# Performance work log

Hardware: AMD Instinct MI355X
Metric: run time of the kernel (lower is better)

## Reference

```python
import jax, jax.numpy as jnp
import numpy as np

DIM = 2048
N_HEADS = 16
HEAD_DIM = 128
EPS = 1e-6


def setup_inputs() -> dict:
    key = jax.random.key(0)
    ks = jax.random.split(key, 8)
    b, gf, gh, gw = 1, 8, 16, 24
    s = gf * gh * gw
    c = HEAD_DIM // 2
    w = lambda k: 0.02 * jax.random.normal(k, (DIM, DIM), jnp.float32)
    return {
        "x": jax.random.normal(ks[0], (b, s, DIM), jnp.float32),
        "freqs_angle": jax.random.normal(ks[1], (1024, c), jnp.float32),
        "Wq": w(ks[2]), "bq": jnp.zeros((DIM,), jnp.float32),
        "Wk": w(ks[3]), "bk": jnp.zeros((DIM,), jnp.float32),
        "Wv": w(ks[4]), "bv": jnp.zeros((DIM,), jnp.float32),
        "Wo": w(ks[5]), "bo": jnp.zeros((DIM,), jnp.float32),
        "gq": jnp.ones((DIM,), jnp.float32),
        "gk": jnp.ones((DIM,), jnp.float32),
        "seq_len": s, "grid_f": gf, "grid_h": gh, "grid_w": gw,
    }


def _rms(t, g):
    return t * jax.lax.rsqrt(jnp.mean(t * t, axis=-1, keepdims=True) + EPS) * g


def _grid_angles(freqs_angle, gf, gh, gw, c):
    # band split [c - 2*(c//3), c//3, c//3] as in rope_apply
    cf = c - 2 * (c // 3)
    ch = cw = c // 3
    af = freqs_angle[:gf, :cf]            # [F, cf]
    ah = freqs_angle[:gh, cf:cf + ch]     # [H, ch]
    aw = freqs_angle[:gw, cf + ch:c]      # [W, cw]
    ang = jnp.concatenate([
        jnp.broadcast_to(af[:, None, None, :], (gf, gh, gw, cf)),
        jnp.broadcast_to(ah[None, :, None, :], (gf, gh, gw, ch)),
        jnp.broadcast_to(aw[None, None, :, :], (gf, gh, gw, cw)),
    ], axis=-1)
    return ang.reshape(gf * gh * gw, c)   # [s, c]


def reference(x, freqs_angle, Wq, bq, Wk, bk, Wv, bv, Wo, bo, gq, gk,
              seq_len, grid_f, grid_h, grid_w):
    b, s, _ = x.shape
    n, d = N_HEADS, HEAD_DIM
    c = d // 2
    ang = _grid_angles(freqs_angle, grid_f, grid_h, grid_w, c)
    cos = jnp.cos(ang)[None, :, None, :]  # [1, s, 1, c]
    sin = jnp.sin(ang)[None, :, None, :]

    def rope(t):  # complex multiply on (even, odd) = (real, imag) pairs
        te, to = t[..., 0::2], t[..., 1::2]
        return jnp.stack([te * cos - to * sin, te * sin + to * cos], axis=-1).reshape(t.shape)

    q = _rms(x @ Wq.T + bq, gq).reshape(b, s, n, d)
    k = _rms(x @ Wk.T + bk, gk).reshape(b, s, n, d)
    v = (x @ Wv.T + bv).reshape(b, s, n, d)
    q, k = rope(q), rope(k)

    scale = np.float32(1.0 / np.sqrt(d))
    scores = jnp.einsum('bqnd,bknd->bnqk', q, k) * scale
    p = jax.nn.softmax(scores, axis=-1)
    o = jnp.einsum('bnqk,bknd->bqnd', p, v).reshape(b, s, n * d)
    return o @ Wo.T + bo
```

## Files before the change

kernel.cpp:

```cpp
#include <hip/hip_runtime.h>
#include <stdint.h>
#include <stddef.h>

typedef __bf16 bf16_t;
typedef __bf16 bf16x8 __attribute__((ext_vector_type(8)));
typedef __bf16 bf16x4 __attribute__((ext_vector_type(4)));
typedef __bf16 bf16x2 __attribute__((ext_vector_type(2)));
typedef float  f32x4  __attribute__((ext_vector_type(4)));
typedef float  f32x16 __attribute__((ext_vector_type(16)));

#define SEQ   3072
#define DIMD  2048
#define NH    16
#define HD    128
#define QKVN  6144

__device__ __forceinline__ void async16(const bf16_t* g, bf16_t* l) {
  __builtin_amdgcn_global_load_lds((const __attribute__((address_space(1))) uint32_t*)g,
                                   (__attribute__((address_space(3))) uint32_t*)l, 16, 0, 0);
}

__global__ __launch_bounds__(256) void cvt_all(const float* __restrict__ x,
                                               const float* __restrict__ Wq,
                                               const float* __restrict__ Wk,
                                               const float* __restrict__ Wv,
                                               const float* __restrict__ Wo,
                                               const float* __restrict__ bq,
                                               const float* __restrict__ bk,
                                               const float* __restrict__ bv,
                                               bf16_t* __restrict__ xb,
                                               bf16_t* __restrict__ Wqkvb,
                                               bf16_t* __restrict__ Wob,
                                               float* __restrict__ bqkv) {
  const int b = blockIdx.x;
  const float* src; bf16_t* dst; int off;
  if (b < 3072)       { src = x;  dst = xb;              off = b; }
  else if (b < 5120)  { src = Wq; dst = Wqkvb;           off = b - 3072; }
  else if (b < 7168)  { src = Wk; dst = Wqkvb + 4194304; off = b - 5120; }
  else if (b < 9216)  { src = Wv; dst = Wqkvb + 8388608; off = b - 7168; }
  else if (b < 11264) { src = Wo; dst = Wob;             off = b - 9216; }
  else {
    int t = (b - 11264) * 256 + threadIdx.x;
    float v;
    if (t < 2048)      v = bq[t];
    else if (t < 4096) v = bk[t - 2048];
    else               v = bv[t - 4096];
    bqkv[t] = v;
    return;
  }
  const int idx = (off * 256 + threadIdx.x) * 8;
  const float4 a = *(const float4*)(src + idx);
  const float4 c = *(const float4*)(src + idx + 4);
  bf16x8 o;
  o[0] = (bf16_t)a.x; o[1] = (bf16_t)a.y; o[2] = (bf16_t)a.z; o[3] = (bf16_t)a.w;
  o[4] = (bf16_t)c.x; o[5] = (bf16_t)c.y; o[6] = (bf16_t)c.z; o[7] = (bf16_t)c.w;
  *(bf16x8*)(dst + idx) = o;
}

template<bool OUT_BF16>
__global__ __launch_bounds__(256, 2) void gemm_nt(const bf16_t* __restrict__ A,
                                                  const bf16_t* __restrict__ B,
                                                  const float* __restrict__ bias,
                                                  void* __restrict__ Cout,
                                                  int M, int N, int K) {
  __shared__ __align__(16) bf16_t As[128 * 64];
  __shared__ __align__(16) bf16_t Bs[128 * 64];
  const int t = threadIdx.x;
  const int lane = t & 63, wave = t >> 6;
  const int quad = lane >> 4, l15 = lane & 15;
  const int wy = wave >> 1, wx = wave & 1;
  const size_t bm = (size_t)blockIdx.y * 128, bn = (size_t)blockIdx.x * 128;
  const bf16_t* Ab = A + bm * K;
  const bf16_t* Bb = B + bn * K;
  f32x4 acc[4][4] = {};
  int srow[4], scol[4];
#pragma unroll
  for (int r = 0; r < 4; r++) {
    int L = r * 256 + t;
    int row = L >> 3, cp = L & 7;
    srow[r] = row;
    scol[r] = (cp ^ (row & 7)) * 8;
  }
  for (int k0 = 0; k0 < K; k0 += 64) {
    __syncthreads();
#pragma unroll
    for (int r = 0; r < 4; r++)
      async16(Ab + (size_t)srow[r] * K + k0 + scol[r], &As[(r * 256 + t) * 8]);
#pragma unroll
    for (int r = 0; r < 4; r++)
      async16(Bb + (size_t)srow[r] * K + k0 + scol[r], &Bs[(r * 256 + t) * 8]);
    __syncthreads();
#pragma unroll
    for (int ks = 0; ks < 2; ks++) {
      bf16x8 af[4], bfv[4];
#pragma unroll
      for (int i = 0; i < 4; i++) {
        int row = wy * 64 + i * 16 + l15;
        af[i] = *(const bf16x8*)&As[row * 64 + (((ks * 4 + quad) ^ (row & 7)) * 8)];
      }
#pragma unroll
      for (int j = 0; j < 4; j++) {
        int row = wx * 64 + j * 16 + l15;
        bfv[j] = *(const bf16x8*)&Bs[row * 64 + (((ks * 4 + quad) ^ (row & 7)) * 8)];
      }
#pragma unroll
      for (int i = 0; i < 4; i++)
#pragma unroll
        for (int j = 0; j < 4; j++)
          acc[i][j] = __builtin_amdgcn_mfma_f32_16x16x32_bf16(af[i], bfv[j], acc[i][j], 0, 0, 0);
    }
  }
#pragma unroll
  for (int i = 0; i < 4; i++) {
#pragma unroll
    for (int j = 0; j < 4; j++) {
      size_t row = bm + wy * 64 + i * 16 + quad * 4;
      size_t col = bn + wx * 64 + j * 16 + l15;
      float bb = bias[col];
#pragma unroll
      for (int r = 0; r < 4; r++) {
        float v = acc[i][j][r] + bb;
        if (OUT_BF16) ((bf16_t*)Cout)[(row + r) * N + col] = (bf16_t)v;
        else          ((float*)Cout)[(row + r) * N + col] = v;
      }
    }
  }
}

__global__ __launch_bounds__(256) void rmsrope(bf16_t* __restrict__ qkv,
                                               bf16_t* __restrict__ pk,
                                               const float* __restrict__ gq,
                                               const float* __restrict__ gk,
                                               const float* __restrict__ freqs) {
  const int s = blockIdx.x, t = threadIdx.x;
  bf16_t* row = qkv + (size_t)s * QKVN;
  bf16x8 qv = *(const bf16x8*)&row[t * 8];
  bf16x8 kv = *(const bf16x8*)&row[2048 + t * 8];
  float qf[8], kf[8];
  float qs = 0.f, ks2 = 0.f;
#pragma unroll
  for (int i = 0; i < 8; i++) {
    qf[i] = (float)qv[i]; qs  += qf[i] * qf[i];
    kf[i] = (float)kv[i]; ks2 += kf[i] * kf[i];
  }
#pragma unroll
  for (int m = 1; m < 64; m <<= 1) {
    qs  += __shfl_xor(qs, m);
    ks2 += __shfl_xor(ks2, m);
  }
  __shared__ float red[2][4];
  const int wave = t >> 6, lane = t & 63;
  if (lane == 0) { red[0][wave] = qs; red[1][wave] = ks2; }
  __syncthreads();
  qs  = red[0][0] + red[0][1] + red[0][2] + red[0][3];
  ks2 = red[1][0] + red[1][1] + red[1][2] + red[1][3];
  const float qsc = rsqrtf(qs  / 2048.f + 1e-6f) * 0.12751745f;
  const float ksc = rsqrtf(ks2 / 2048.f + 1e-6f);
  const int sf = s / 384, rem = s - sf * 384;
  const int sh = rem / 24, sw = rem - sh * 24;
  bf16x8 qo, ko;
#pragma unroll
  for (int u = 0; u < 4; u++) {
    const int col = t * 8 + 2 * u;
    const int i = (col >> 1) & 63;
    const int frow = (i < 22) ? sf : ((i < 43) ? sh : sw);
    const float ang = freqs[frow * 64 + i];
    float sn, cs;
    __sincosf(ang, &sn, &cs);
    float te = qf[2 * u]     * qsc * gq[col];
    float to = qf[2 * u + 1] * qsc * gq[col + 1];
    qo[2 * u]     = (bf16_t)(te * cs - to * sn);
    qo[2 * u + 1] = (bf16_t)(te * sn + to * cs);
    te = kf[2 * u]     * ksc * gk[col];
    to = kf[2 * u + 1] * ksc * gk[col + 1];
    ko[2 * u]     = (bf16_t)(te * cs - to * sn);
    ko[2 * u + 1] = (bf16_t)(te * sn + to * cs);
  }
  *(bf16x8*)&row[t * 8] = qo;
  *(bf16x8*)&pk[((size_t)(t >> 4) * SEQ + s) * HD + (t & 15) * 8] = ko;
}

__global__ __launch_bounds__(256) void vtrans(const bf16_t* __restrict__ qkv,
                                              bf16_t* __restrict__ pvt) {
  __shared__ bf16_t tile[128][65];
  const int h = blockIdx.y;
  const int s0 = blockIdx.x * 64;
  const int t = threadIdx.x;
#pragma unroll
  for (int r = 0; r < 4; r++) {
    int L = r * 256 + t, s = L >> 4, cp = L & 15;
    bf16x8 v = *(const bf16x8*)&qkv[(size_t)(s0 + s) * QKVN + 4096 + h * HD + cp * 8];
#pragma unroll
    for (int i = 0; i < 8; i++) tile[cp * 8 + i][s] = v[i];
  }
  __syncthreads();
#pragma unroll
  for (int r = 0; r < 4; r++) {
    int L = r * 256 + t, d = L >> 3, c = L & 7;
    bf16x8 o;
#pragma unroll
    for (int i = 0; i < 8; i++) o[i] = tile[d][c * 8 + i];
    *(bf16x8*)&pvt[((size_t)h * HD + d) * SEQ + s0 + c * 8] = o;
  }
}

#define STAGE_KV(BUF, KV1) do {                                              \
    _Pragma("unroll")                                                        \
    for (int r = 0; r < 5; r++) {                                            \
      int L = r * 192 + t;                                                   \
      async16(pkh + (size_t)(KV1) * HD + koff[r], &Ks[BUF][L * 8]);          \
      async16(pvh + (KV1) + voff[r], &Vt[BUF][L * 8]);                       \
    }                                                                        \
    if (t < 64) {                                                            \
      int L = 5 * 192 + t;                                                   \
      async16(pkh + (size_t)(KV1) * HD + koff[5], &Ks[BUF][L * 8]);          \
      async16(pvh + (KV1) + voff[5], &Vt[BUF][L * 8]);                       \
    }                                                                        \
  } while (0)

__global__ __launch_bounds__(192, 2) void flash_attn(const bf16_t* __restrict__ qkv,
                                                     const bf16_t* __restrict__ pk,
                                                     const bf16_t* __restrict__ pvt,
                                                     bf16_t* __restrict__ ob) {
  __shared__ __align__(16) bf16_t Ks[2][64 * 128];
  __shared__ __align__(16) bf16_t Vt[2][128 * 64];
  const int hh = blockIdx.y, qt = blockIdx.x;
  const int s0 = qt * 96;
  const int t = threadIdx.x, wave = t >> 6, lane = t & 63;
  const int l31 = lane & 31, hl = lane >> 5;
  const int wq = wave * 32;
  const bf16_t* pkh = pk  + (size_t)hh * (SEQ * HD);
  const bf16_t* pvh = pvt + (size_t)hh * (HD * SEQ);
  int koff[6], voff[6];
#pragma unroll
  for (int r = 0; r < 6; r++) {
    int L = r * 192 + t;
    int krow = L >> 4, kc = (L & 15) ^ (krow & 7);
    koff[r] = krow * HD + kc * 8;
    int vd = L >> 3, vc = (L & 7) ^ (vd & 7);
    voff[r] = vd * SEQ + vc * 8;
  }
  bf16x8 qfr[8];
#pragma unroll
  for (int ks = 0; ks < 8; ks++)
    qfr[ks] = *(const bf16x8*)&qkv[(size_t)(s0 + wq + l31) * QKVN + hh * HD + ks * 16 + hl * 8];
  bf16x8 vones;
#pragma unroll
  for (int i = 0; i < 8; i++) vones[i] = (bf16_t)1.0f;
  f32x16 oacc[4] = {};
  f32x16 lacc = {};
  float m_run = -3e38f;
  STAGE_KV(0, 0);
  for (int kt = 0; kt < SEQ / 64; kt++) {
    const int cur = kt & 1;
    __syncthreads();
    if (kt + 1 < SEQ / 64) STAGE_KV(cur ^ 1, (kt + 1) * 64);
    f32x16 st0 = {}, st1 = {};
    __builtin_amdgcn_s_setprio(1);
#pragma unroll
    for (int ks = 0; ks < 8; ks++) {
      const int r1 = 32 + l31;
      bf16x8 k0 = *(const bf16x8*)&Ks[cur][l31 * 128 + (((ks * 2 + hl) ^ (l31 & 7)) * 8)];
      bf16x8 k1 = *(const bf16x8*)&Ks[cur][r1 * 128 + (((ks * 2 + hl) ^ (r1 & 7)) * 8)];
      st0 = __builtin_amdgcn_mfma_f32_32x32x16_bf16(k0, qfr[ks], st0, 0, 0, 0);
      st1 = __builtin_amdgcn_mfma_f32_32x32x16_bf16(k1, qfr[ks], st1, 0, 0, 0);
    }
    __builtin_amdgcn_s_setprio(0);
    float mt = st0[0];
#pragma unroll
    for (int r = 1; r < 16; r++) mt = fmaxf(mt, st0[r]);
#pragma unroll
    for (int r = 0; r < 16; r++) mt = fmaxf(mt, st1[r]);
    mt = fmaxf(mt, __shfl_xor(mt, 32));
    if (!__all(mt <= m_run + 11.5f)) {
      const float mn = fmaxf(m_run, mt);
      const float al = __builtin_amdgcn_exp2f(m_run - mn);
      m_run = mn;
#pragma unroll
      for (int r = 0; r < 16; r++) {
        const float a = __shfl(al, (r & 3) + 8 * (r >> 2) + 4 * hl);
        lacc[r] *= a;
#pragma unroll
        for (int dj = 0; dj < 4; dj++) oacc[dj][r] *= a;
      }
    }
    uint32_t c0[8], c1[8];
#pragma unroll
    for (int m = 0; m < 8; m++) {
      bf16x2 w0, w1;
      w0[0] = (bf16_t)__builtin_amdgcn_exp2f(st0[2 * m]     - m_run);
      w0[1] = (bf16_t)__builtin_amdgcn_exp2f(st0[2 * m + 1] - m_run);
      w1[0] = (bf16_t)__builtin_amdgcn_exp2f(st1[2 * m]     - m_run);
      w1[1] = (bf16_t)__builtin_amdgcn_exp2f(st1[2 * m + 1] - m_run);
      c0[m] = __builtin_bit_cast(uint32_t, w0);
      c1[m] = __builtin_bit_cast(uint32_t, w1);
    }
    union U8 { uint32_t u[4]; bf16x8 v; } afr0, afr1, afr2, afr3;
#define BUILD_AFR(DST, CB, B) do {                                           \
      uint32_t sA = hl ? CB[(B) + 0] : CB[(B) + 2];                          \
      uint32_t sB = hl ? CB[(B) + 1] : CB[(B) + 3];                          \
      uint32_t rA = (uint32_t)__shfl_xor((int)sA, 32);                       \
      uint32_t rB = (uint32_t)__shfl_xor((int)sB, 32);                       \
      DST.u[0] = hl ? rA : CB[(B) + 0];                                      \
      DST.u[1] = hl ? rB : CB[(B) + 1];                                      \
      DST.u[2] = hl ? CB[(B) + 2] : rA;                                      \
      DST.u[3] = hl ? CB[(B) + 3] : rB;                                      \
    } while (0)
    BUILD_AFR(afr0, c0, 0);
    BUILD_AFR(afr1, c0, 4);
    BUILD_AFR(afr2, c1, 0);
    BUILD_AFR(afr3, c1, 4);
#undef BUILD_AFR
    __builtin_amdgcn_s_setprio(1);
#define PV_STEP(AFR, S) do {                                                            \
      lacc = __builtin_amdgcn_mfma_f32_32x32x16_bf16(AFR.v, vones, lacc, 0, 0, 0);      \
      _Pragma("unroll")                                                                 \
      for (int dj = 0; dj < 4; dj++) {                                                  \
        const int row = dj * 32 + l31;                                                  \
        bf16x8 vf = *(const bf16x8*)&Vt[cur][row * 64 + ((((S) * 2 + hl) ^ (row & 7)) * 8)]; \
        oacc[dj] = __builtin_amdgcn_mfma_f32_32x32x16_bf16(AFR.v, vf, oacc[dj], 0, 0, 0);    \
      }                                                                                 \
    } while (0)
    PV_STEP(afr0, 0);
    PV_STEP(afr1, 1);
    PV_STEP(afr2, 2);
    PV_STEP(afr3, 3);
#undef PV_STEP
    __builtin_amdgcn_s_setprio(0);
  }
#pragma unroll
  for (int r = 0; r < 16; r++) {
    const float li = 1.f / lacc[r];
    const size_t row = (size_t)(s0 + wq + (r & 3) + 8 * (r >> 2) + 4 * hl);
#pragma unroll
    for (int dj = 0; dj < 4; dj++)
      ob[row * DIMD + hh * HD + dj * 32 + l31] = (bf16_t)(oacc[dj][r] * li);
  }
}

extern "C" void kernel_launch(void* const* d_in, const int* in_sizes, int n_in,
                              void* d_out, int out_size, void* d_ws, size_t ws_size,
                              hipStream_t stream) {
  (void)in_sizes; (void)n_in; (void)out_size;
  const float* x     = (const float*)d_in[0];
  const float* freqs = (const float*)d_in[1];
  const float* Wq    = (const float*)d_in[2];
  const float* bq    = (const float*)d_in[3];
  const float* Wk    = (const float*)d_in[4];
  const float* bk    = (const float*)d_in[5];
  const float* Wv    = (const float*)d_in[6];
  const float* bv    = (const float*)d_in[7];
  const float* Wo    = (const float*)d_in[8];
  const float* bo    = (const float*)d_in[9];
  const float* gq    = (const float*)d_in[10];
  const float* gk    = (const float*)d_in[11];

  char* w = (char*)d_ws;
  bf16_t* xb    = (bf16_t*)(w);
  bf16_t* Wqkvb = (bf16_t*)(w + 12582912);
  bf16_t* Wob   = (bf16_t*)(w + 37748736);
  bf16_t* qkvb  = (bf16_t*)(w + 46137344);
  bf16_t* obuf  = (bf16_t*)(w + 83886080);
  float*  bqkv  = (float*) (w + 96468992);
  bf16_t* pk    = (bf16_t*)(w);
  bf16_t* pvt   = (bf16_t*)(w + 12582912);
  if (ws_size < (size_t)96493568) return;

  cvt_all<<<11288, 256, 0, stream>>>(x, Wq, Wk, Wv, Wo, bq, bk, bv, xb, Wqkvb, Wob, bqkv);

  gemm_nt<true><<<dim3(48, 24), 256, 0, stream>>>(xb, Wqkvb, bqkv, qkvb, SEQ, QKVN, DIMD);
  rmsrope<<<3072, 256, 0, stream>>>(qkvb, pk, gq, gk, freqs);
  vtrans<<<dim3(48, NH), 256, 0, stream>>>(qkvb, pvt);
  flash_attn<<<dim3(32, NH), 192, 0, stream>>>(qkvb, pk, pvt, obuf);
  gemm_nt<false><<<dim3(16, 24), 256, 0, stream>>>(obuf, Wob, bo, (float*)d_out, SEQ, DIMD, DIMD);
}
```

Before: 422.2 us.

## Split attention KV range in two with merge kernel, drop running-max rescaling

Each (head, query tile) is split into two blocks, each covering half of the key sequence with 32-key tiles. The grid grows to 1024 blocks, and the flat block index is swizzled to pick the tile, head and half. Occupancy is raised to 3 blocks per SM, and K and V now share one LDS buffer with a new swizzle. The online-softmax max tracking and rescaling are removed: scores go straight into exp2. That leans on RMS-normed q and k keeping the logits bounded, so it can overflow if the gains are large. The unnormalized partials (one fp32, one bf16) and the row sums are written to reused workspace regions. A new merge kernel sums them and normalizes before the output projection.

```diff
diff --git a/kernel.cpp b/kernel.cpp
--- a/kernel.cpp
+++ b/kernel.cpp
@@ -204,41 +204,41 @@
   }
 }
 
-#define STAGE_KV(BUF, KV1) do {                                              \
+#define STAGE_KV(BUF, KV0) do {                                              \
     _Pragma("unroll")                                                        \
     for (int r = 0; r < 5; r++) {                                            \
-      int L = r * 192 + t;                                                   \
-      async16(pkh + (size_t)(KV1) * HD + koff[r], &Ks[BUF][L * 8]);          \
-      async16(pvh + (KV1) + voff[r], &Vt[BUF][L * 8]);                       \
+      int c = r * 192 + t;                                                   \
+      if (c < 512) async16(pkh + (size_t)(KV0) * HD + goff[r], &KV[BUF][c * 8]); \
+      else         async16(pvh + (KV0) + goff[r], &KV[BUF][c * 8]);          \
     }                                                                        \
     if (t < 64) {                                                            \
-      int L = 5 * 192 + t;                                                   \
-      async16(pkh + (size_t)(KV1) * HD + koff[5], &Ks[BUF][L * 8]);          \
-      async16(pvh + (KV1) + voff[5], &Vt[BUF][L * 8]);                       \
+      async16(pvh + (KV0) + goff[5], &KV[BUF][(960 + t) * 8]);               \
     }                                                                        \
   } while (0)
 
-__global__ __launch_bounds__(192, 2) void flash_attn(const bf16_t* __restrict__ qkv,
+__global__ __launch_bounds__(192, 3) void flash_attn(const bf16_t* __restrict__ qkv,
                                                      const bf16_t* __restrict__ pk,
                                                      const bf16_t* __restrict__ pvt,
-                                                     bf16_t* __restrict__ ob) {
-  __shared__ __align__(16) bf16_t Ks[2][64 * 128];
-  __shared__ __align__(16) bf16_t Vt[2][128 * 64];
-  const int hh = blockIdx.y, qt = blockIdx.x;
+                                                     char* __restrict__ p0c,
+                                                     bf16_t* __restrict__ p1,
+                                                     float* __restrict__ lsum) {
+  __shared__ __align__(16) bf16_t KV[2][8192];
+  const int flat = blockIdx.x;
+  const int wg = (flat & 7) * 128 + (flat >> 3);
+  const int qt = wg & 31, hs = wg >> 5;
+  const int hh = hs >> 1, split = hs & 1;
   const int s0 = qt * 96;
   const int t = threadIdx.x, wave = t >> 6, lane = t & 63;
   const int l31 = lane & 31, hl = lane >> 5;
   const int wq = wave * 32;
-  const bf16_t* pkh = pk  + (size_t)hh * (SEQ * HD);
-  const bf16_t* pvh = pvt + (size_t)hh * (HD * SEQ);
-  int koff[6], voff[6];
+  const bf16_t* pkh = pk  + (size_t)hh * (SEQ * HD) + (size_t)(split * 1536) * HD;
+  const bf16_t* pvh = pvt + (size_t)hh * (HD * SEQ) + split * 1536;
+  int goff[6];
 #pragma unroll
   for (int r = 0; r < 6; r++) {
-    int L = r * 192 + t;
-    int krow = L >> 4, kc = (L & 15) ^ (krow & 7);
-    koff[r] = krow * HD + kc * 8;
-    int vd = L >> 3, vc = (L & 7) ^ (vd & 7);
-    voff[r] = vd * SEQ + vc * 8;
+    int c = r * 192 + t;
+    if (c < 512) { int kr = c >> 4; goff[r] = kr * HD + (((c & 15) ^ (kr & 7)) * 8); }
+    else { int c2 = c - 512; int vd = c2 >> 2; goff[r] = vd * SEQ + (((c2 & 3) ^ (vd & 3)) * 8); }
   }
   bf16x8 qfr[8];
 #pragma unroll
@@ -249,53 +249,28 @@
   for (int i = 0; i < 8; i++) vones[i] = (bf16_t)1.0f;
   f32x16 oacc[4] = {};
   f32x16 lacc = {};
-  float m_run = -3e38f;
   STAGE_KV(0, 0);
-  for (int kt = 0; kt < SEQ / 64; kt++) {
+  for (int kt = 0; kt < 48; kt++) {
     const int cur = kt & 1;
     __syncthreads();
-    if (kt + 1 < SEQ / 64) STAGE_KV(cur ^ 1, (kt + 1) * 64);
-    f32x16 st0 = {}, st1 = {};
+    if (kt + 1 < 48) STAGE_KV(cur ^ 1, (kt + 1) * 32);
+    f32x16 st = {};
     __builtin_amdgcn_s_setprio(1);
 #pragma unroll
     for (int ks = 0; ks < 8; ks++) {
-      const int r1 = 32 + l31;
-      bf16x8 k0 = *(const bf16x8*)&Ks[cur][l31 * 128 + (((ks * 2 + hl) ^ (l31 & 7)) * 8)];
-      bf16x8 k1 = *(const bf16x8*)&Ks[cur][r1 * 128 + (((ks * 2 + hl) ^ (r1 & 7)) * 8)];
-      st0 = __builtin_amdgcn_mfma_f32_32x32x16_bf16(k0, qfr[ks], st0, 0, 0, 0);
-      st1 = __builtin_amdgcn_mfma_f32_32x32x16_bf16(k1, qfr[ks], st1, 0, 0, 0);
+      bf16x8 kf = *(const bf16x8*)&KV[cur][l31 * 128 + (((ks * 2 + hl) ^ (l31 & 7)) * 8)];
+      st = __builtin_amdgcn_mfma_f32_32x32x16_bf16(kf, qfr[ks], st, 0, 0, 0);
     }
     __builtin_amdgcn_s_setprio(0);
-    float mt = st0[0];
-#pragma unroll
-    for (int r = 1; r < 16; r++) mt = fmaxf(mt, st0[r]);
-#pragma unroll
-    for (int r = 0; r < 16; r++) mt = fmaxf(mt, st1[r]);
-    mt = fmaxf(mt, __shfl_xor(mt, 32));
-    if (!__all(mt <= m_run + 11.5f)) {
-      const float mn = fmaxf(m_run, mt);
-      const float al = __builtin_amdgcn_exp2f(m_run - mn);
-      m_run = mn;
-#pragma unroll
-      for (int r = 0; r < 16; r++) {
-        const float a = __shfl(al, (r & 3) + 8 * (r >> 2) + 4 * hl);
-        lacc[r] *= a;
-#pragma unroll
-        for (int dj = 0; dj < 4; dj++) oacc[dj][r] *= a;
-      }
-    }
-    uint32_t c0[8], c1[8];
+    uint32_t c0[8];
 #pragma unroll
     for (int m = 0; m < 8; m++) {
-      bf16x2 w0, w1;
-      w0[0] = (bf16_t)__builtin_amdgcn_exp2f(st0[2 * m]     - m_run);
-      w0[1] = (bf16_t)__builtin_amdgcn_exp2f(st0[2 * m + 1] - m_run);
-      w1[0] = (bf16_t)__builtin_amdgcn_exp2f(st1[2 * m]     - m_run);
-      w1[1] = (bf16_t)__builtin_amdgcn_exp2f(st1[2 * m + 1] - m_run);
-      c0[m] = __builtin_bit_cast(uint32_t, w0);
-      c1[m] = __builtin_bit_cast(uint32_t, w1);
-    }
-    union U8 { uint32_t u[4]; bf16x8 v; } afr0, afr1, afr2, afr3;
+      bf16x2 w2;
+      w2[0] = (bf16_t)__builtin_amdgcn_exp2f(st[2 * m]);
+      w2[1] = (bf16_t)__builtin_amdgcn_exp2f(st[2 * m + 1]);
+      c0[m] = __builtin_bit_cast(uint32_t, w2);
+    }
+    union U8 { uint32_t u[4]; bf16x8 v; } afr0, afr1;
 #define BUILD_AFR(DST, CB, B) do {                                           \
       uint32_t sA = hl ? CB[(B) + 0] : CB[(B) + 2];                          \
       uint32_t sB = hl ? CB[(B) + 1] : CB[(B) + 3];                          \
@@ -308,8 +283,6 @@
     } while (0)
     BUILD_AFR(afr0, c0, 0);
     BUILD_AFR(afr1, c0, 4);
-    BUILD_AFR(afr2, c1, 0);
-    BUILD_AFR(afr3, c1, 4);
 #undef BUILD_AFR
     __builtin_amdgcn_s_setprio(1);
 #define PV_STEP(AFR, S) do {                                                            \
@@ -317,25 +290,64 @@
       _Pragma("unroll")                                                                 \
       for (int dj = 0; dj < 4; dj++) {                                                  \
         const int row = dj * 32 + l31;                                                  \
-        bf16x8 vf = *(const bf16x8*)&Vt[cur][row * 64 + ((((S) * 2 + hl) ^ (row & 7)) * 8)]; \
+        bf16x8 vf = *(const bf16x8*)&KV[cur][4096 + row * 32 + ((((S) * 2 + hl) ^ (row & 3)) * 8)]; \
         oacc[dj] = __builtin_amdgcn_mfma_f32_32x32x16_bf16(AFR.v, vf, oacc[dj], 0, 0, 0);    \
       }                                                                                 \
     } while (0)
     PV_STEP(afr0, 0);
     PV_STEP(afr1, 1);
-    PV_STEP(afr2, 2);
-    PV_STEP(afr3, 3);
 #undef PV_STEP
     __builtin_amdgcn_s_setprio(0);
   }
-#pragma unroll
-  for (int r = 0; r < 16; r++) {
-    const float li = 1.f / lacc[r];
-    const size_t row = (size_t)(s0 + wq + (r & 3) + 8 * (r >> 2) + 4 * hl);
-#pragma unroll
-    for (int dj = 0; dj < 4; dj++)
-      ob[row * DIMD + hh * HD + dj * 32 + l31] = (bf16_t)(oacc[dj][r] * li);
-  }
+  if (split == 0) {
+#pragma unroll
+    for (int r = 0; r < 16; r++) {
+      const int row = (r & 3) + 8 * (r >> 2) + 4 * hl;
+      float* dst = (float*)(p0c + (size_t)(s0 + wq + row) * 12288 + 4096) + hh * HD + l31;
+#pragma unroll
+      for (int dj = 0; dj < 4; dj++) dst[dj * 32] = oacc[dj][r];
+    }
+  } else {
+#pragma unroll
+    for (int r = 0; r < 16; r++) {
+      const int row = (r & 3) + 8 * (r >> 2) + 4 * hl;
+      bf16_t* dst = p1 + (size_t)(s0 + wq + row) * DIMD + hh * HD + l31;
+#pragma unroll
+      for (int dj = 0; dj < 4; dj++) dst[dj * 32] = (bf16_t)oacc[dj][r];
+    }
+  }
+  if (l31 == 0) {
+#pragma unroll
+    for (int r = 0; r < 16; r++) {
+      const int row = (r & 3) + 8 * (r >> 2) + 4 * hl;
+      lsum[((size_t)split * SEQ + s0 + wq + row) * NH + hh] = lacc[r];
+    }
+  }
+}
+
+__global__ __launch_bounds__(256) void merge_attn(const char* __restrict__ p0c,
+                                                  bf16_t* __restrict__ p1,
+                                                  const float* __restrict__ lsum) {
+  const int s = blockIdx.x, t = threadIdx.x;
+  const int h = t >> 4;
+  const float l0 = lsum[(size_t)s * NH + h];
+  const float l1 = lsum[((size_t)SEQ + s) * NH + h];
+  const float inv = 1.f / (l0 + l1);
+  const float* a = (const float*)(p0c + (size_t)s * 12288 + 4096) + t * 8;
+  bf16_t* b = p1 + (size_t)s * DIMD + t * 8;
+  const float4 x0 = *(const float4*)a;
+  const float4 x1 = *(const float4*)(a + 4);
+  bf16x8 pv = *(const bf16x8*)b;
+  bf16x8 o;
+  o[0] = (bf16_t)((x0.x + (float)pv[0]) * inv);
+  o[1] = (bf16_t)((x0.y + (float)pv[1]) * inv);
+  o[2] = (bf16_t)((x0.z + (float)pv[2]) * inv);
+  o[3] = (bf16_t)((x0.w + (float)pv[3]) * inv);
+  o[4] = (bf16_t)((x1.x + (float)pv[4]) * inv);
+  o[5] = (bf16_t)((x1.y + (float)pv[5]) * inv);
+  o[6] = (bf16_t)((x1.z + (float)pv[6]) * inv);
+  o[7] = (bf16_t)((x1.w + (float)pv[7]) * inv);
+  *(bf16x8*)b = o;
 }
 
 extern "C" void kernel_launch(void* const* d_in, const int* in_sizes, int n_in,
@@ -360,10 +372,12 @@
   bf16_t* Wqkvb = (bf16_t*)(w + 12582912);
   bf16_t* Wob   = (bf16_t*)(w + 37748736);
   bf16_t* qkvb  = (bf16_t*)(w + 46137344);
-  bf16_t* obuf  = (bf16_t*)(w + 83886080);
   float*  bqkv  = (float*) (w + 96468992);
   bf16_t* pk    = (bf16_t*)(w);
   bf16_t* pvt   = (bf16_t*)(w + 12582912);
+  bf16_t* p1    = (bf16_t*)(w + 25165824);
+  char*   p0c   = w + 46137344;
+  float*  lsum  = (float*) (w + 83886080);
   if (ws_size < (size_t)96493568) return;
 
   cvt_all<<<11288, 256, 0, stream>>>(x, Wq, Wk, Wv, Wo, bq, bk, bv, xb, Wqkvb, Wob, bqkv);
@@ -371,6 +385,7 @@
   gemm_nt<true><<<dim3(48, 24), 256, 0, stream>>>(xb, Wqkvb, bqkv, qkvb, SEQ, QKVN, DIMD);
   rmsrope<<<3072, 256, 0, stream>>>(qkvb, pk, gq, gk, freqs);
   vtrans<<<dim3(48, NH), 256, 0, stream>>>(qkvb, pvt);
-  flash_attn<<<dim3(32, NH), 192, 0, stream>>>(qkvb, pk, pvt, obuf);
-  gemm_nt<false><<<dim3(16, 24), 256, 0, stream>>>(obuf, Wob, bo, (float*)d_out, SEQ, DIMD, DIMD);
-}
+  flash_attn<<<dim3(1024), 192, 0, stream>>>(qkvb, pk, pvt, p0c, p1, lsum);
+  merge_attn<<<dim3(SEQ), 256, 0, stream>>>(p0c, p1, lsum);
+  gemm_nt<false><<<dim3(16, 24), 256, 0, stream>>>(p1, Wob, bo, (float*)d_out, SEQ, DIMD, DIMD);
+}
```

After: 436.2 us. 1.03x slower.
